# Kernel optimization log

Measured on AMD Instinct MI355X. Metric: run time of the kernel, lower is better.

## Reference

```python
import jax, jax.numpy as jnp
import numpy as np

V, E, SH, H = 30000, 1024, 2048, 1024   # vocab, emb_size, ses_hid_size, hid_size
B, T = 64, 50
PAD = 10003
H2 = 2 * H  # GRU hidden size


def setup_inputs() -> dict:
    key = jax.random.key(0)
    ks = jax.random.split(key, 12)
    s = 0.02
    emb_W = jax.random.normal(ks[2], (V, E), jnp.float32) * s
    emb_W = emb_W.at[PAD].set(0.0)  # padding_idx row is zero
    return {
        "ses_encoding": jax.random.normal(ks[0], (B, 1, SH), jnp.float32),
        "x": jax.random.randint(ks[1], (B, T), 0, V),
        "emb_W": emb_W,
        "gru_Wih": jax.random.normal(ks[3], (3 * H2, E), jnp.float32) * s,
        "gru_Whh": jax.random.normal(ks[4], (3 * H2, H2), jnp.float32) * s,
        "gru_bih": jax.random.normal(ks[5], (3 * H2,), jnp.float32) * s,
        "gru_bhh": jax.random.normal(ks[6], (3 * H2,), jnp.float32) * s,
        "lin1_W": jax.random.normal(ks[7], (H, SH), jnp.float32) * s,
        "lin1_b": jax.random.normal(ks[8], (H,), jnp.float32) * s,
        "lin2_W": jax.random.normal(ks[9], (E, H2), jnp.float32) * s,
        "lin2_b": jax.random.normal(ks[10], (E,), jnp.float32) * s,
        "out_W": jax.random.normal(ks[11], (V, E), jnp.float32) * s,
    }


def reference(ses_encoding, x, emb_W, gru_Wih, gru_Whh, gru_bih, gru_bhh,
              lin1_W, lin1_b, lin2_W, lin2_b, out_W):
    # ses_encoding: [B,1,SH] -> tanh(lin1) -> [B,1,H] -> view [1,B,H] -> [B,H]
    ses = jnp.tanh(jnp.einsum('bos,hs->boh', ses_encoding, lin1_W) + lin1_b)
    ses_enc = ses.reshape(B, H)  # [B, H]

    toks = x.T  # [T, B], teacher-forced inputs
    tok_next = jnp.concatenate([x[:, 1:], jnp.zeros((B, 1), x.dtype)], axis=1).T  # [T, B]
    has_next = jnp.arange(T) < (T - 1)  # [T]

    def step(h, xs):
        tok, nxt, hn = xs  # tok: [B]
        emb = jnp.where((tok == PAD)[:, None], 0.0, emb_W[tok])  # [B, E] (dropout=eval identity)
        hcat = jnp.concatenate([h, ses_enc], axis=-1)  # [B, 2H]
        gi = emb @ gru_Wih.T + gru_bih    # [B, 6H]
        gh = hcat @ gru_Whh.T + gru_bhh   # [B, 6H]
        i_r, i_z, i_n = jnp.split(gi, 3, axis=-1)
        h_r, h_z, h_n = jnp.split(gh, 3, axis=-1)
        r = jax.nn.sigmoid(i_r + h_r)
        z = jax.nn.sigmoid(i_z + h_z)
        n = jnp.tanh(i_n + r * h_n)
        h_full = (1.0 - z) * n + z * hcat     # [B, 2H]
        h_next = h_full[:, :H]                # keep first hid_size half
        hid_o = h_full @ lin2_W.T + lin2_b + emb  # [B, E]
        logits = hid_o @ out_W.T              # [B, V]
        logp = jax.nn.log_softmax(logits, axis=-1)
        ll = jnp.where(hn, logp[jnp.arange(B), nxt], 0.0)  # [B]
        return h_next, (logits, ll)

    _, (all_logits, all_ll) = jax.lax.scan(step, ses_enc, (toks, tok_next, has_next))
    dec_o = jnp.transpose(all_logits, (1, 0, 2))  # [B, T, V]
    log_l = jnp.sum(all_ll, axis=0)               # [B]
    return dec_o, log_l
```

## Files before the change

### kernel.cpp

```cpp
#include <hip/hip_runtime.h>
#include <hip/hip_bf16.h>
#include <stdint.h>

#define VV   30000
#define EE   1024
#define SHH  2048
#define HH   1024
#define H2   2048
#define G3   6144
#define BB   64
#define TT   50
#define PADT 10003
#define MM   3200
#define NPAD 30080
#define RBLK 64
#define PNB  (NPAD / 64)

typedef __bf16 bf16;
typedef bf16  bf16x8 __attribute__((ext_vector_type(8)));
typedef bf16  bf16x4v __attribute__((ext_vector_type(4)));
typedef float f32x4 __attribute__((ext_vector_type(4)));

__device__ __forceinline__ void async16(void* lds_base, const void* gsrc) {
    __builtin_amdgcn_global_load_lds(
        (const __attribute__((address_space(1))) void*)gsrc,
        (__attribute__((address_space(3))) void*)lds_base, 16, 0, 0);
}

__device__ __forceinline__ int xcd_swizzle(int lin, int nwg) {
    int q = nwg >> 3, r = nwg & 7;
    int x = lin & 7, o = lin >> 3;
    return (x < r ? x * (q + 1) : r * (q + 1) + (x - r) * q) + o;
}

__device__ __forceinline__ float sigmoidf_(float x) {
    return 1.f / (1.f + __expf(-x));
}

__global__ __launch_bounds__(256) void k_conv(bf16* dst, const float* src, int n) {
    int i = (blockIdx.x * 256 + threadIdx.x) * 4;
    if (i + 3 >= n) return;
    float4 v = *(const float4*)&src[i];
    bf16x4v o; o[0] = (bf16)v.x; o[1] = (bf16)v.y; o[2] = (bf16)v.z; o[3] = (bf16)v.w;
    *(bf16x4v*)&dst[i] = o;
}

__global__ __launch_bounds__(256) void k_conv_outw(bf16* dst, const float* src) {
    int row = blockIdx.x;
    int c = threadIdx.x * 4;
    bf16x4v o;
    if (row < VV) {
        float4 v = *(const float4*)&src[(size_t)row * EE + c];
        o[0] = (bf16)v.x; o[1] = (bf16)v.y; o[2] = (bf16)v.z; o[3] = (bf16)v.w;
    } else {
        o[0] = (bf16)0.f; o[1] = (bf16)0.f; o[2] = (bf16)0.f; o[3] = (bf16)0.f;
    }
    *(bf16x4v*)&dst[(size_t)row * EE + c] = o;
}

__global__ __launch_bounds__(256) void k_conv_whhhi(bf16* dst, const float* whh) {
    int d = blockIdx.x;
    int cblk = d / 192, rem = d % 192, g = rem / 64, s = rem % 64;
    const float* srow = whh + (size_t)(g * H2 + 1024 + cblk * 64 + s) * H2;
    int c = threadIdx.x * 4;
    float4 v = *(const float4*)&srow[c];
    bf16x4v o; o[0] = (bf16)v.x; o[1] = (bf16)v.y; o[2] = (bf16)v.z; o[3] = (bf16)v.w;
    *(bf16x4v*)&dst[(size_t)d * HH + c] = o;
}

__global__ __launch_bounds__(256) void k_embed(const int* x, const float* embW, bf16* out) {
    int i = blockIdx.x;
    int t = i >> 6, b = i & 63;
    int tok = x[b * TT + t];
    int e = threadIdx.x * 4;
    bf16x4v o;
    if (tok == PADT) {
        o[0] = (bf16)0.f; o[1] = (bf16)0.f; o[2] = (bf16)0.f; o[3] = (bf16)0.f;
    } else {
        float4 v = *(const float4*)&embW[(size_t)tok * EE + e];
        o[0] = (bf16)v.x; o[1] = (bf16)v.y; o[2] = (bf16)v.z; o[3] = (bf16)v.w;
    }
    *(bf16x4v*)&out[(size_t)i * EE + e] = o;
}

template<int KIND>
__global__ __launch_bounds__(256)
void sgemm64(const float* __restrict__ A, const float* __restrict__ Bm,
             const float* __restrict__ bias, float* __restrict__ Of,
             bf16* __restrict__ Ob, bf16* __restrict__ Ob2,
             int N, int K, int lda, int ldb, int koff, int ldo, int ldo2) {
    int n0 = blockIdx.x * 64;
    int tid = threadIdx.x;
    int tr = tid >> 4, tc = tid & 15;
    __shared__ float As[64][33];
    __shared__ float Bs[64][33];
    float acc[4][4] = {};
    for (int k0 = 0; k0 < K; k0 += 32) {
        #pragma unroll
        for (int q = 0; q < 8; ++q) {
            int p = q * 256 + tid; int r = p >> 5, kk = p & 31;
            As[r][kk] = A[(size_t)r * lda + k0 + kk];
            Bs[r][kk] = Bm[(size_t)(n0 + r) * ldb + koff + k0 + kk];
        }
        __syncthreads();
        #pragma unroll
        for (int kk = 0; kk < 32; ++kk) {
            float a4[4], b4[4];
            #pragma unroll
            for (int i = 0; i < 4; i++) a4[i] = As[tr * 4 + i][kk];
            #pragma unroll
            for (int j = 0; j < 4; j++) b4[j] = Bs[tc * 4 + j][kk];
            #pragma unroll
            for (int i = 0; i < 4; i++)
                #pragma unroll
                for (int j = 0; j < 4; j++) acc[i][j] += a4[i] * b4[j];
        }
        __syncthreads();
    }
    #pragma unroll
    for (int i = 0; i < 4; i++)
        #pragma unroll
        for (int j = 0; j < 4; j++) {
            int row = tr * 4 + i, col = n0 + tc * 4 + j;
            float v = acc[i][j] + bias[col];
            if (KIND == 0) {
                v = tanhf(v);
                Of[(size_t)row * N + col] = v;
                Ob[(size_t)row * ldo + col] = (bf16)v;
                Ob2[(size_t)row * ldo2 + col] = (bf16)v;
            } else {
                Of[(size_t)row * N + col] = v;
            }
        }
}

template<int KIND>
__global__ __launch_bounds__(256)
void gemm128(const bf16* __restrict__ A, const bf16* __restrict__ Bm,
             void* __restrict__ Cout, const float* __restrict__ bias,
             const bf16* __restrict__ addend, float* __restrict__ pm,
             float* __restrict__ ps, int N, int K, int lda, int ldb, int Nreal) {
    int nwg = gridDim.x * gridDim.y;
    int lin = blockIdx.y * gridDim.x + blockIdx.x;
    int wg = xcd_swizzle(lin, nwg);
    int bx = wg % gridDim.x, by = wg / gridDim.x;
    const int n0 = bx * 128;
    const int m0 = by * 128;
    const int tid = threadIdx.x;
    const int w = tid >> 6, l = tid & 63;
    const int wr = w >> 1, wc = w & 1;
    __shared__ bf16 As[2][128 * 32];
    __shared__ bf16 Bs[2][128 * 32];
    f32x4 acc[4][4] = {};
    const int lrow = l >> 2;
    const int lk = (l & 3) * 8;

    auto stage = [&](int buf, int kt) {
        #pragma unroll
        for (int q = 0; q < 2; ++q) {
            int ch = w * 2 + q;
            async16(&As[buf][ch * 512], A + (size_t)(m0 + ch * 16 + lrow) * lda + kt + lk);
            async16(&Bs[buf][ch * 512], Bm + (size_t)(n0 + ch * 16 + lrow) * ldb + kt + lk);
        }
    };

    stage(0, 0);
    __syncthreads();
    const int nk = K >> 5;
    for (int ki = 0; ki < nk; ++ki) {
        const int cur = ki & 1;
        if (ki + 1 < nk) stage(cur ^ 1, (ki + 1) << 5);
        bf16x8 af[4], bfr[4];
        #pragma unroll
        for (int mi = 0; mi < 4; mi++)
            af[mi] = *(const bf16x8*)&As[cur][(wr * 64 + mi * 16 + (l & 15)) * 32 + (l >> 4) * 8];
        #pragma unroll
        for (int ni = 0; ni < 4; ni++)
            bfr[ni] = *(const bf16x8*)&Bs[cur][(wc * 64 + ni * 16 + (l & 15)) * 32 + (l >> 4) * 8];
        #pragma unroll
        for (int mi = 0; mi < 4; mi++)
            #pragma unroll
            for (int ni = 0; ni < 4; ni++)
                acc[mi][ni] = __builtin_amdgcn_mfma_f32_16x16x32_bf16(af[mi], bfr[ni], acc[mi][ni], 0, 0, 0);
        __syncthreads();
    }
    #pragma unroll
    for (int mi = 0; mi < 4; mi++)
        #pragma unroll
        for (int ni = 0; ni < 4; ni++) {
            int row0 = m0 + wr * 64 + mi * 16 + (l >> 4) * 4;
            int col = n0 + wc * 64 + ni * 16 + (l & 15);
            f32x4 v = acc[mi][ni];
            #pragma unroll
            for (int r = 0; r < 4; r++) {
                int rr = row0 + r;
                float xv = v[r];
                if constexpr (KIND == 0 || KIND == 1) xv += bias[col];
                if constexpr (KIND == 1) xv += (float)addend[(size_t)rr * N + col];
                if constexpr (KIND == 2) {
                    if (col < Nreal) {
                        int t = rr >> 6, b = rr & 63;
                        __builtin_nontemporal_store(
                            xv, &((float*)Cout)[((size_t)(b * TT + t)) * VV + col]);
                    }
                } else {
                    ((bf16*)Cout)[(size_t)rr * N + col] = (bf16)xv;
                }
            }
        }
    if constexpr (KIND == 2) {
        #pragma unroll
        for (int mi = 0; mi < 4; mi++) {
            #pragma unroll
            for (int r = 0; r < 4; r++) {
                float m = -1e30f, s = 0.f;
                #pragma unroll
                for (int ni = 0; ni < 4; ni++) {
                    int col = n0 + wc * 64 + ni * 16 + (l & 15);
                    if (col < Nreal) {
                        float v = acc[mi][ni][r];
                        float M = fmaxf(m, v);
                        s = s * __expf(m - M) + __expf(v - M);
                        m = M;
                    }
                }
                #pragma unroll
                for (int off = 1; off < 16; off <<= 1) {
                    float m2 = __shfl_xor(m, off);
                    float s2 = __shfl_xor(s, off);
                    float M = fmaxf(m, m2);
                    s = s * __expf(m - M) + s2 * __expf(m2 - M);
                    m = M;
                }
                if ((l & 15) == 0) {
                    int row = m0 + wr * 64 + mi * 16 + (l >> 4) * 4 + r;
                    size_t pidx = (size_t)row * PNB + (n0 >> 6) + wc;
                    pm[pidx] = m; ps[pidx] = s;
                }
            }
        }
    }
}

__global__ __launch_bounds__(384, 1)
void k_rnn(const float* __restrict__ Whh,
           const bf16* __restrict__ gi_b,
           const float* __restrict__ ghs,
           bf16* __restrict__ hlo,
           bf16* __restrict__ hfx,
           uint32_t* __restrict__ ctr) {
    const int blk = blockIdx.x;
    const int c0 = blk * 16;
    const int tid = threadIdx.x;
    const int wv = tid >> 6;
    const int l  = tid & 63;
    const int g  = wv >> 1;
    const int mh = wv & 1;
    const int lc = l & 15, lk = l >> 4;
    __shared__ char h_lds[131072];
    __shared__ float ghl[3][64][17];

    bf16x8 breg[32];
    {
        const float* wrow = Whh + ((size_t)(g * H2 + c0 + lc)) * H2;
        #pragma unroll
        for (int kt = 0; kt < 32; ++kt) {
            const float* p = wrow + kt * 32 + lk * 8;
            float4 v0 = *(const float4*)p;
            float4 v1 = *(const float4*)(p + 4);
            bf16x8 o;
            o[0] = (bf16)v0.x; o[1] = (bf16)v0.y; o[2] = (bf16)v0.z; o[3] = (bf16)v0.w;
            o[4] = (bf16)v1.x; o[5] = (bf16)v1.y; o[6] = (bf16)v1.z; o[7] = (bf16)v1.w;
            breg[kt] = o;
        }
    }
    float pr[4], pz[4], pn[4];
    if (wv < 4) {
        #pragma unroll
        for (int r = 0; r < 4; ++r) {
            int b = wv * 16 + lk * 4 + r;
            size_t base = (size_t)b * G3 + c0 + lc;
            pr[r] = ghs[base];
            pz[r] = ghs[base + H2];
            pn[r] = ghs[base + 2 * H2];
        }
    }

    for (int t = 0; t < TT; ++t) {
        bf16 qr[4], qz[4], qn[4];
        if (wv < 4) {
            const bf16* gp = gi_b + ((size_t)t * BB) * G3;
            #pragma unroll
            for (int r = 0; r < 4; ++r) {
                int b = wv * 16 + lk * 4 + r;
                size_t base = (size_t)b * G3 + c0 + lc;
                qr[r] = gp[base];
                qz[r] = gp[base + H2];
                qn[r] = gp[base + 2 * H2];
            }
        }

        {
            const uint64_t* hsrc = (const uint64_t*)(hlo + (size_t)t * BB * HH);
            #pragma unroll 1
            for (int i0 = 0; i0 < 44; i0 += 22) {
                uint64_t v[22];
                #pragma unroll
                for (int j = 0; j < 22; ++j) {
                    int idx = (i0 + j) * 384 + tid;
                    if (idx < 16384)
                        v[j] = __hip_atomic_load(hsrc + idx, __ATOMIC_RELAXED,
                                                 __HIP_MEMORY_SCOPE_AGENT);
                }
                #pragma unroll
                for (int j = 0; j < 22; ++j) {
                    int idx = (i0 + j) * 384 + tid;
                    if (idx < 16384) {
                        int byte = idx * 8;
                        int swb = byte ^ (((byte >> 11) & 7) << 4);
                        *(uint64_t*)(h_lds + swb) = v[j];
                    }
                }
            }
        }
        __syncthreads();

        f32x4 acc0 = {}, acc1 = {};
        const int r0 = mh * 32 + lc, r1 = r0 + 16;
        const int sw = (lc & 7) << 4;
        #pragma unroll
        for (int kt = 0; kt < 32; ++kt) {
            int cbyte = kt * 64 + lk * 16;
            bf16x8 a0 = *(const bf16x8*)(h_lds + ((r0 * 2048 + cbyte) ^ sw));
            bf16x8 a1 = *(const bf16x8*)(h_lds + ((r1 * 2048 + cbyte) ^ sw));
            acc0 = __builtin_amdgcn_mfma_f32_16x16x32_bf16(a0, breg[kt], acc0, 0, 0, 0);
            acc1 = __builtin_amdgcn_mfma_f32_16x16x32_bf16(a1, breg[kt], acc1, 0, 0, 0);
        }
        #pragma unroll
        for (int r = 0; r < 4; ++r) {
            ghl[g][mh * 32 + lk * 4 + r][lc]      = acc0[r];
            ghl[g][mh * 32 + 16 + lk * 4 + r][lc] = acc1[r];
        }
        __syncthreads();

        if (wv < 4) {
            #pragma unroll
            for (int r = 0; r < 4; ++r) {
                int b = wv * 16 + lk * 4 + r;
                float hr = ghl[0][b][lc] + pr[r];
                float hz = ghl[1][b][lc] + pz[r];
                float hn = ghl[2][b][lc] + pn[r];
                float rg = sigmoidf_((float)qr[r] + hr);
                float zg = sigmoidf_((float)qz[r] + hz);
                float ng = tanhf((float)qn[r] + rg * hn);
                int hvb = (b * 2048 + (c0 + lc) * 2) ^ ((b & 7) << 4);
                float hv = (float)*(const bf16*)(h_lds + hvb);
                float hf = (1.f - zg) * ng + zg * hv;
                union { bf16 h; uint16_t u; } cv;
                cv.h = (bf16)hf;
                __hip_atomic_store(
                    (uint16_t*)&hlo[((size_t)(t + 1) * BB + b) * HH + c0 + lc],
                    cv.u, __ATOMIC_RELAXED, __HIP_MEMORY_SCOPE_AGENT);
                hfx[((size_t)(t + 1) * BB + b) * H2 + c0 + lc] = cv.h;
            }
        }

        if (t != TT - 1) {
            __syncthreads();
            if (tid == 0) {
                __hip_atomic_fetch_add(&ctr[t], 1u, __ATOMIC_RELAXED, __HIP_MEMORY_SCOPE_AGENT);
                while (__hip_atomic_load(&ctr[t], __ATOMIC_RELAXED, __HIP_MEMORY_SCOPE_AGENT) < RBLK)
                    __builtin_amdgcn_s_sleep(1);
            }
            __syncthreads();
        }
    }
}

__global__ __launch_bounds__(256)
void k_hi(const bf16* __restrict__ hfx_,
          const float* __restrict__ ses_f,
          const bf16* __restrict__ Wrh,
          const bf16* __restrict__ gi_b,
          const float* __restrict__ ghs,
          bf16* __restrict__ hfx_out) {
    const int cblk = blockIdx.x;
    const int t    = blockIdx.y;
    const int tid = threadIdx.x;
    const int w = tid >> 6, l = tid & 63;
    __shared__ bf16 As[64 * 32];
    __shared__ bf16 Bs[192 * 32];
    f32x4 acc[12] = {};
    const int lrow = l >> 2;
    const int lk = (l & 3) * 8;
    const bf16* Abase = hfx_ + ((size_t)t * BB) * H2;
    for (int kt = 0; kt < HH; kt += 32) {
        async16(&As[w * 512], Abase + (size_t)(w * 16 + lrow) * H2 + kt + lk);
        #pragma unroll
        for (int q = 0; q < 3; ++q) {
            int cb = w * 3 + q;
            async16(&Bs[cb * 512], Wrh + (size_t)(cblk * 192 + cb * 16 + lrow) * HH + kt + lk);
        }
        __syncthreads();
        bf16x8 af = *(const bf16x8*)&As[(w * 16 + (l & 15)) * 32 + (l >> 4) * 8];
        #pragma unroll
        for (int j = 0; j < 12; j++) {
            bf16x8 bfj = *(const bf16x8*)&Bs[(j * 16 + (l & 15)) * 32 + (l >> 4) * 8];
            acc[j] = __builtin_amdgcn_mfma_f32_16x16x32_bf16(af, bfj, acc[j], 0, 0, 0);
        }
        __syncthreads();
    }
    #pragma unroll
    for (int jc = 0; jc < 4; jc++) {
        int ch = cblk * 64 + jc * 16 + (l & 15);
        #pragma unroll
        for (int r = 0; r < 4; r++) {
            int b = w * 16 + (l >> 4) * 4 + r;
            size_t gb = (size_t)(t * BB + b) * G3 + 1024 + ch;
            size_t sb = (size_t)b * G3 + 1024 + ch;
            float gr = (float)gi_b[gb];
            float gz = (float)gi_b[gb + H2];
            float gn = (float)gi_b[gb + 2 * H2];
            float hr = acc[jc][r]     + ghs[sb];
            float hz = acc[4 + jc][r] + ghs[sb + H2];
            float hn = acc[8 + jc][r] + ghs[sb + 2 * H2];
            float rg = sigmoidf_(gr + hr);
            float zg = sigmoidf_(gz + hz);
            float ng = tanhf(gn + rg * hn);
            float hv = ses_f[b * HH + ch];
            float hf = (1.f - zg) * ng + zg * hv;
            hfx_out[((size_t)(t + 1) * BB + b) * H2 + HH + ch] = (bf16)hf;
        }
    }
}

__global__ void k_lse(const float* __restrict__ pm, const float* __restrict__ ps,
                      const float* __restrict__ logits, const int* __restrict__ x,
                      float* __restrict__ ll) {
    int row = blockIdx.x;
    int t = row >> 6, b = row & 63;
    int l = threadIdx.x;
    float m = -1e30f, s = 0.f;
    for (int i = l; i < PNB; i += 64) {
        float mi = pm[(size_t)row * PNB + i];
        float si = ps[(size_t)row * PNB + i];
        float M = fmaxf(m, mi);
        s = s * __expf(m - M) + si * __expf(mi - M);
        m = M;
    }
    #pragma unroll
    for (int off = 32; off; off >>= 1) {
        float m2 = __shfl_down(m, off);
        float s2 = __shfl_down(s, off);
        float M = fmaxf(m, m2);
        s = s * __expf(m - M) + s2 * __expf(m2 - M);
        m = M;
    }
    if (l == 0) {
        float v = 0.f;
        if (t < TT - 1) {
            int nxt = x[b * TT + t + 1];
            v = logits[((size_t)(b * TT + t)) * VV + nxt] - (m + __logf(s));
        }
        ll[row] = v;
    }
}

__global__ void k_sumll(const float* __restrict__ ll_ws, float* __restrict__ out) {
    int b = threadIdx.x;
    if (b < BB) {
        float s = 0.f;
        for (int t = 0; t < TT; t++) s += ll_ws[t * BB + b];
        out[b] = s;
    }
}

extern "C" void kernel_launch(void* const* d_in, const int* in_sizes, int n_in,
                              void* d_out, int out_size, void* d_ws, size_t ws_size,
                              hipStream_t stream) {
    const float* ses_encoding = (const float*)d_in[0];
    const int*   x            = (const int*)d_in[1];
    const float* emb_W        = (const float*)d_in[2];
    const float* gru_Wih      = (const float*)d_in[3];
    const float* gru_Whh      = (const float*)d_in[4];
    const float* gru_bih      = (const float*)d_in[5];
    const float* gru_bhh      = (const float*)d_in[6];
    const float* lin1_W       = (const float*)d_in[7];
    const float* lin1_b       = (const float*)d_in[8];
    const float* lin2_W       = (const float*)d_in[9];
    const float* lin2_b       = (const float*)d_in[10];
    const float* out_W        = (const float*)d_in[11];

    char* W = (char*)d_ws;
    size_t off = 0;
    auto take = [&](size_t bytes) { void* p = W + off; off += (bytes + 255) & ~(size_t)255; return p; };

    float* ses_f32 = (float*)take((size_t)BB * HH * 4);
    bf16* Wih_b    = (bf16*)take((size_t)G3 * EE * 2);
    bf16* Wrh_b    = (bf16*)take((size_t)3072 * HH * 2);
    bf16* lin2_b16 = (bf16*)take((size_t)EE * H2 * 2);
    bf16* outW_b   = (bf16*)take((size_t)NPAD * EE * 2);
    bf16* emb_b    = (bf16*)take((size_t)MM * EE * 2);
    bf16* gi_b     = (bf16*)take((size_t)MM * G3 * 2);
    float* ghs     = (float*)take((size_t)BB * G3 * 4);
    bf16* hlo      = (bf16*)take((size_t)(TT + 1) * BB * HH * 2);
    bf16* hfx      = (bf16*)take((size_t)(TT + 1) * BB * H2 * 2);
    bf16* hido_b   = (bf16*)take((size_t)MM * EE * 2);
    float* ll_ws   = (float*)take((size_t)MM * 4);
    float* pm      = (float*)take((size_t)MM * PNB * 4);
    float* ps      = (float*)take((size_t)MM * PNB * 4);
    uint32_t* ctr  = (uint32_t*)take((size_t)TT * 4);

    hipMemsetAsync(ctr, 0, (size_t)TT * 4, stream);

    k_conv<<<(G3 * EE) / 1024, 256, 0, stream>>>(Wih_b, gru_Wih, G3 * EE);
    k_conv<<<(EE * H2) / 1024, 256, 0, stream>>>(lin2_b16, lin2_W, EE * H2);
    k_conv_outw<<<NPAD, 256, 0, stream>>>(outW_b, out_W);
    k_conv_whhhi<<<3072, 256, 0, stream>>>(Wrh_b, gru_Whh);
    k_embed<<<MM, 256, 0, stream>>>(x, emb_W, emb_b);

    sgemm64<0><<<HH / 64, 256, 0, stream>>>(ses_encoding, lin1_W, lin1_b, ses_f32,
                                            hfx, hlo, HH, SHH, SHH, SHH, 0, H2, HH);
    sgemm64<1><<<G3 / 64, 256, 0, stream>>>(ses_f32, gru_Whh, gru_bhh, ghs, nullptr,
                                            nullptr, G3, HH, HH, H2, HH, 0, 0);

    gemm128<0><<<dim3(G3 / 128, MM / 128), 256, 0, stream>>>(
        emb_b, Wih_b, gi_b, gru_bih, nullptr, nullptr, nullptr, G3, EE, EE, EE, 0);

    k_rnn<<<RBLK, 384, 0, stream>>>(gru_Whh, gi_b, ghs, hlo, hfx, ctr);

    k_hi<<<dim3(16, TT), 256, 0, stream>>>(hfx, ses_f32, Wrh_b, gi_b, ghs, hfx);

    gemm128<1><<<dim3(EE / 128, MM / 128), 256, 0, stream>>>(
        hfx + (size_t)BB * H2, lin2_b16, hido_b, lin2_b, emb_b, nullptr, nullptr,
        EE, H2, H2, H2, 0);

    gemm128<2><<<dim3(NPAD / 128, MM / 128), 256, 0, stream>>>(
        hido_b, outW_b, d_out, nullptr, nullptr, pm, ps, NPAD, EE, EE, EE, VV);

    k_lse<<<MM, 64, 0, stream>>>(pm, ps, (const float*)d_out, x, ll_ws);
    k_sumll<<<1, 64, 0, stream>>>(ll_ws, (float*)d_out + (size_t)BB * TT * VV);
}
```

Measured before the change: 1.508 ms.

## Fuse upper-half GRU gate kernel into recurrent kernel as overlapping worker blocks

The separate k_hi launch is merged into k_rnn. 192 extra blocks poll the per-step counters and compute the upper-half hidden GEMM and gates for each finished timestep while the 64 recurrent blocks continue with later steps. The aim is to hide k_hi's work behind the serial recurrence and remove one launch. The cost is that the worker blocks share the GPU with the recurrent blocks and spin on flags. Only 4 of their 6 waves do work, and both block types reserve the large LDS allocation, so each takes a whole CU.

```diff
diff --git a/kernel.cpp b/kernel.cpp
--- a/kernel.cpp
+++ b/kernel.cpp
@@ -14,6 +14,7 @@
 #define MM   3200
 #define NPAD 30080
 #define RBLK 64
+#define HIBLK 192
 #define PNB  (NPAD / 64)
 
 typedef __bf16 bf16;
@@ -248,188 +249,203 @@
            const float* __restrict__ ghs,
            bf16* __restrict__ hlo,
            bf16* __restrict__ hfx,
-           uint32_t* __restrict__ ctr) {
-    const int blk = blockIdx.x;
-    const int c0 = blk * 16;
+           uint32_t* __restrict__ ctr,
+           const float* __restrict__ ses_f,
+           const bf16* __restrict__ Wrh) {
+    __shared__ char smem[144128];
     const int tid = threadIdx.x;
     const int wv = tid >> 6;
     const int l  = tid & 63;
-    const int g  = wv >> 1;
-    const int mh = wv & 1;
-    const int lc = l & 15, lk = l >> 4;
-    __shared__ char h_lds[131072];
-    __shared__ float ghl[3][64][17];
-
-    bf16x8 breg[32];
-    {
-        const float* wrow = Whh + ((size_t)(g * H2 + c0 + lc)) * H2;
-        #pragma unroll
-        for (int kt = 0; kt < 32; ++kt) {
-            const float* p = wrow + kt * 32 + lk * 8;
-            float4 v0 = *(const float4*)p;
-            float4 v1 = *(const float4*)(p + 4);
-            bf16x8 o;
-            o[0] = (bf16)v0.x; o[1] = (bf16)v0.y; o[2] = (bf16)v0.z; o[3] = (bf16)v0.w;
-            o[4] = (bf16)v1.x; o[5] = (bf16)v1.y; o[6] = (bf16)v1.z; o[7] = (bf16)v1.w;
-            breg[kt] = o;
-        }
-    }
-    float pr[4], pz[4], pn[4];
-    if (wv < 4) {
-        #pragma unroll
-        for (int r = 0; r < 4; ++r) {
-            int b = wv * 16 + lk * 4 + r;
-            size_t base = (size_t)b * G3 + c0 + lc;
-            pr[r] = ghs[base];
-            pz[r] = ghs[base + H2];
-            pn[r] = ghs[base + 2 * H2];
-        }
-    }
-
-    for (int t = 0; t < TT; ++t) {
-        bf16 qr[4], qz[4], qn[4];
+
+    if (blockIdx.x < RBLK) {
+        char* h_lds = smem;
+        float (*ghl)[64][17] = (float(*)[64][17])(smem + 131072);
+        const int blk = blockIdx.x;
+        const int c0 = blk * 16;
+        const int g  = wv >> 1;
+        const int mh = wv & 1;
+        const int lc = l & 15, lk = l >> 4;
+
+        bf16x8 breg[32];
+        {
+            const float* wrow = Whh + ((size_t)(g * H2 + c0 + lc)) * H2;
+            #pragma unroll
+            for (int kt = 0; kt < 32; ++kt) {
+                const float* p = wrow + kt * 32 + lk * 8;
+                float4 v0 = *(const float4*)p;
+                float4 v1 = *(const float4*)(p + 4);
+                bf16x8 o;
+                o[0] = (bf16)v0.x; o[1] = (bf16)v0.y; o[2] = (bf16)v0.z; o[3] = (bf16)v0.w;
+                o[4] = (bf16)v1.x; o[5] = (bf16)v1.y; o[6] = (bf16)v1.z; o[7] = (bf16)v1.w;
+                breg[kt] = o;
+            }
+        }
+        float pr[4], pz[4], pn[4];
         if (wv < 4) {
-            const bf16* gp = gi_b + ((size_t)t * BB) * G3;
             #pragma unroll
             for (int r = 0; r < 4; ++r) {
                 int b = wv * 16 + lk * 4 + r;
                 size_t base = (size_t)b * G3 + c0 + lc;
-                qr[r] = gp[base];
-                qz[r] = gp[base + H2];
-                qn[r] = gp[base + 2 * H2];
-            }
-        }
-
-        {
-            const uint64_t* hsrc = (const uint64_t*)(hlo + (size_t)t * BB * HH);
-            #pragma unroll 1
-            for (int i0 = 0; i0 < 44; i0 += 22) {
-                uint64_t v[22];
+                pr[r] = ghs[base];
+                pz[r] = ghs[base + H2];
+                pn[r] = ghs[base + 2 * H2];
+            }
+        }
+
+        for (int t = 0; t < TT; ++t) {
+            bf16 qr[4], qz[4], qn[4];
+            if (wv < 4) {
+                const bf16* gp = gi_b + ((size_t)t * BB) * G3;
                 #pragma unroll
-                for (int j = 0; j < 22; ++j) {
-                    int idx = (i0 + j) * 384 + tid;
-                    if (idx < 16384)
-                        v[j] = __hip_atomic_load(hsrc + idx, __ATOMIC_RELAXED,
-                                                 __HIP_MEMORY_SCOPE_AGENT);
-                }
+                for (int r = 0; r < 4; ++r) {
+                    int b = wv * 16 + lk * 4 + r;
+                    size_t base = (size_t)b * G3 + c0 + lc;
+                    qr[r] = gp[base];
+                    qz[r] = gp[base + H2];
+                    qn[r] = gp[base + 2 * H2];
+                }
+            }
+            {
+                const uint64_t* hsrc = (const uint64_t*)(hlo + (size_t)t * BB * HH);
+                #pragma unroll 1
+                for (int i0 = 0; i0 < 44; i0 += 22) {
+                    uint64_t v[22];
+                    #pragma unroll
+                    for (int j = 0; j < 22; ++j) {
+                        int idx = (i0 + j) * 384 + tid;
+                        if (idx < 16384)
+                            v[j] = __hip_atomic_load(hsrc + idx, __ATOMIC_RELAXED,
+                                                     __HIP_MEMORY_SCOPE_AGENT);
+                    }
+                    #pragma unroll
+                    for (int j = 0; j < 22; ++j) {
+                        int idx = (i0 + j) * 384 + tid;
+                        if (idx < 16384) {
+                            int byte = idx * 8;
+                            int swb = byte ^ (((byte >> 11) & 7) << 4);
+                            *(uint64_t*)(h_lds + swb) = v[j];
+                        }
+                    }
+                }
+            }
+            __syncthreads();
+
+            f32x4 acc0 = {}, acc1 = {};
+            const int r0 = mh * 32 + lc, r1 = r0 + 16;
+            const int sw = (lc & 7) << 4;
+            #pragma unroll
+            for (int kt = 0; kt < 32; ++kt) {
+                int cbyte = kt * 64 + lk * 16;
+                bf16x8 a0 = *(const bf16x8*)(h_lds + ((r0 * 2048 + cbyte) ^ sw));
+                bf16x8 a1 = *(const bf16x8*)(h_lds + ((r1 * 2048 + cbyte) ^ sw));
+                acc0 = __builtin_amdgcn_mfma_f32_16x16x32_bf16(a0, breg[kt], acc0, 0, 0, 0);
+                acc1 = __builtin_amdgcn_mfma_f32_16x16x32_bf16(a1, breg[kt], acc1, 0, 0, 0);
+            }
+            #pragma unroll
+            for (int r = 0; r < 4; ++r) {
+                ghl[g][mh * 32 + lk * 4 + r][lc]      = acc0[r];
+                ghl[g][mh * 32 + 16 + lk * 4 + r][lc] = acc1[r];
+            }
+            __syncthreads();
+
+            if (wv < 4) {
                 #pragma unroll
-                for (int j = 0; j < 22; ++j) {
-                    int idx = (i0 + j) * 384 + tid;
-                    if (idx < 16384) {
-                        int byte = idx * 8;
-                        int swb = byte ^ (((byte >> 11) & 7) << 4);
-                        *(uint64_t*)(h_lds + swb) = v[j];
-                    }
-                }
-            }
-        }
-        __syncthreads();
-
-        f32x4 acc0 = {}, acc1 = {};
-        const int r0 = mh * 32 + lc, r1 = r0 + 16;
-        const int sw = (lc & 7) << 4;
-        #pragma unroll
-        for (int kt = 0; kt < 32; ++kt) {
-            int cbyte = kt * 64 + lk * 16;
-            bf16x8 a0 = *(const bf16x8*)(h_lds + ((r0 * 2048 + cbyte) ^ sw));
-            bf16x8 a1 = *(const bf16x8*)(h_lds + ((r1 * 2048 + cbyte) ^ sw));
-            acc0 = __builtin_amdgcn_mfma_f32_16x16x32_bf16(a0, breg[kt], acc0, 0, 0, 0);
-            acc1 = __builtin_amdgcn_mfma_f32_16x16x32_bf16(a1, breg[kt], acc1, 0, 0, 0);
-        }
-        #pragma unroll
-        for (int r = 0; r < 4; ++r) {
-            ghl[g][mh * 32 + lk * 4 + r][lc]      = acc0[r];
-            ghl[g][mh * 32 + 16 + lk * 4 + r][lc] = acc1[r];
-        }
-        __syncthreads();
-
-        if (wv < 4) {
-            #pragma unroll
-            for (int r = 0; r < 4; ++r) {
-                int b = wv * 16 + lk * 4 + r;
-                float hr = ghl[0][b][lc] + pr[r];
-                float hz = ghl[1][b][lc] + pz[r];
-                float hn = ghl[2][b][lc] + pn[r];
-                float rg = sigmoidf_((float)qr[r] + hr);
-                float zg = sigmoidf_((float)qz[r] + hz);
-                float ng = tanhf((float)qn[r] + rg * hn);
-                int hvb = (b * 2048 + (c0 + lc) * 2) ^ ((b & 7) << 4);
-                float hv = (float)*(const bf16*)(h_lds + hvb);
-                float hf = (1.f - zg) * ng + zg * hv;
-                union { bf16 h; uint16_t u; } cv;
-                cv.h = (bf16)hf;
-                __hip_atomic_store(
-                    (uint16_t*)&hlo[((size_t)(t + 1) * BB + b) * HH + c0 + lc],
-                    cv.u, __ATOMIC_RELAXED, __HIP_MEMORY_SCOPE_AGENT);
-                hfx[((size_t)(t + 1) * BB + b) * H2 + c0 + lc] = cv.h;
-            }
-        }
-
-        if (t != TT - 1) {
+                for (int r = 0; r < 4; ++r) {
+                    int b = wv * 16 + lk * 4 + r;
+                    float hr = ghl[0][b][lc] + pr[r];
+                    float hz = ghl[1][b][lc] + pz[r];
+                    float hn = ghl[2][b][lc] + pn[r];
+                    float rg = sigmoidf_((float)qr[r] + hr);
+                    float zg = sigmoidf_((float)qz[r] + hz);
+                    float ng = tanhf((float)qn[r] + rg * hn);
+                    int hvb = (b * 2048 + (c0 + lc) * 2) ^ ((b & 7) << 4);
+                    float hv = (float)*(const bf16*)(h_lds + hvb);
+                    float hf = (1.f - zg) * ng + zg * hv;
+                    union { bf16 h; uint16_t u; } cv;
+                    cv.h = (bf16)hf;
+                    __hip_atomic_store(
+                        (uint16_t*)&hlo[((size_t)(t + 1) * BB + b) * HH + c0 + lc],
+                        cv.u, __ATOMIC_RELAXED, __HIP_MEMORY_SCOPE_AGENT);
+                    hfx[((size_t)(t + 1) * BB + b) * H2 + c0 + lc] = cv.h;
+                }
+            }
+
+            if (t != TT - 1) {
+                __syncthreads();
+                if (tid == 0) {
+                    __hip_atomic_fetch_add(&ctr[t], 1u, __ATOMIC_RELAXED, __HIP_MEMORY_SCOPE_AGENT);
+                    while (__hip_atomic_load(&ctr[t], __ATOMIC_RELAXED, __HIP_MEMORY_SCOPE_AGENT) < RBLK)
+                        __builtin_amdgcn_s_sleep(1);
+                }
+                __syncthreads();
+            }
+        }
+    } else {
+        bf16* As = (bf16*)smem;
+        bf16* Bs = (bf16*)(smem + 4096);
+        const int w = wv;
+        const int lrow = l >> 2;
+        const int lk8 = (l & 3) * 8;
+
+        for (int item = (int)blockIdx.x - RBLK; item < TT * 16; item += HIBLK) {
+            const int t = item >> 4, cblk = item & 15;
+            if (t > 0 && tid == 0) {
+                while (__hip_atomic_load(&ctr[t - 1], __ATOMIC_RELAXED, __HIP_MEMORY_SCOPE_AGENT) < RBLK)
+                    __builtin_amdgcn_s_sleep(32);
+            }
             __syncthreads();
-            if (tid == 0) {
-                __hip_atomic_fetch_add(&ctr[t], 1u, __ATOMIC_RELAXED, __HIP_MEMORY_SCOPE_AGENT);
-                while (__hip_atomic_load(&ctr[t], __ATOMIC_RELAXED, __HIP_MEMORY_SCOPE_AGENT) < RBLK)
-                    __builtin_amdgcn_s_sleep(1);
+
+            f32x4 acc[12] = {};
+            for (int kt = 0; kt < HH; kt += 32) {
+                if (w < 4) {
+                    const uint64_t* src = (const uint64_t*)(
+                        hlo + ((size_t)t * BB + w * 16 + lrow) * HH + kt + lk8);
+                    uint64_t v0 = __hip_atomic_load(src, __ATOMIC_RELAXED, __HIP_MEMORY_SCOPE_AGENT);
+                    uint64_t v1 = __hip_atomic_load(src + 1, __ATOMIC_RELAXED, __HIP_MEMORY_SCOPE_AGENT);
+                    uint64_t* dst = (uint64_t*)((char*)As + w * 1024 + l * 16);
+                    dst[0] = v0; dst[1] = v1;
+                    #pragma unroll
+                    for (int q = 0; q < 3; ++q) {
+                        int cb = w * 3 + q;
+                        async16(&Bs[cb * 512], Wrh + (size_t)(cblk * 192 + cb * 16 + lrow) * HH + kt + lk8);
+                    }
+                }
+                __syncthreads();
+                if (w < 4) {
+                    bf16x8 af = *(const bf16x8*)&As[(w * 16 + (l & 15)) * 32 + (l >> 4) * 8];
+                    #pragma unroll
+                    for (int j = 0; j < 12; j++) {
+                        bf16x8 bfj = *(const bf16x8*)&Bs[(j * 16 + (l & 15)) * 32 + (l >> 4) * 8];
+                        acc[j] = __builtin_amdgcn_mfma_f32_16x16x32_bf16(af, bfj, acc[j], 0, 0, 0);
+                    }
+                }
+                __syncthreads();
+            }
+            if (w < 4) {
+                #pragma unroll
+                for (int jc = 0; jc < 4; jc++) {
+                    int ch = cblk * 64 + jc * 16 + (l & 15);
+                    #pragma unroll
+                    for (int r = 0; r < 4; r++) {
+                        int b = w * 16 + (l >> 4) * 4 + r;
+                        size_t gb = (size_t)(t * BB + b) * G3 + 1024 + ch;
+                        size_t sb = (size_t)b * G3 + 1024 + ch;
+                        float gr = (float)gi_b[gb];
+                        float gz = (float)gi_b[gb + H2];
+                        float gn = (float)gi_b[gb + 2 * H2];
+                        float hr = acc[jc][r]     + ghs[sb];
+                        float hz = acc[4 + jc][r] + ghs[sb + H2];
+                        float hn = acc[8 + jc][r] + ghs[sb + 2 * H2];
+                        float rg = sigmoidf_(gr + hr);
+                        float zg = sigmoidf_(gz + hz);
+                        float ng = tanhf(gn + rg * hn);
+                        float hv = ses_f[b * HH + ch];
+                        float hf = (1.f - zg) * ng + zg * hv;
+                        hfx[((size_t)(t + 1) * BB + b) * H2 + HH + ch] = (bf16)hf;
+                    }
+                }
             }
             __syncthreads();
-        }
-    }
-}
-
-__global__ __launch_bounds__(256)
-void k_hi(const bf16* __restrict__ hfx_,
-          const float* __restrict__ ses_f,
-          const bf16* __restrict__ Wrh,
-          const bf16* __restrict__ gi_b,
-          const float* __restrict__ ghs,
-          bf16* __restrict__ hfx_out) {
-    const int cblk = blockIdx.x;
-    const int t    = blockIdx.y;
-    const int tid = threadIdx.x;
-    const int w = tid >> 6, l = tid & 63;
-    __shared__ bf16 As[64 * 32];
-    __shared__ bf16 Bs[192 * 32];
-    f32x4 acc[12] = {};
-    const int lrow = l >> 2;
-    const int lk = (l & 3) * 8;
-    const bf16* Abase = hfx_ + ((size_t)t * BB) * H2;
-    for (int kt = 0; kt < HH; kt += 32) {
-        async16(&As[w * 512], Abase + (size_t)(w * 16 + lrow) * H2 + kt + lk);
-        #pragma unroll
-        for (int q = 0; q < 3; ++q) {
-            int cb = w * 3 + q;
-            async16(&Bs[cb * 512], Wrh + (size_t)(cblk * 192 + cb * 16 + lrow) * HH + kt + lk);
-        }
-        __syncthreads();
-        bf16x8 af = *(const bf16x8*)&As[(w * 16 + (l & 15)) * 32 + (l >> 4) * 8];
-        #pragma unroll
-        for (int j = 0; j < 12; j++) {
-            bf16x8 bfj = *(const bf16x8*)&Bs[(j * 16 + (l & 15)) * 32 + (l >> 4) * 8];
-            acc[j] = __builtin_amdgcn_mfma_f32_16x16x32_bf16(af, bfj, acc[j], 0, 0, 0);
-        }
-        __syncthreads();
-    }
-    #pragma unroll
-    for (int jc = 0; jc < 4; jc++) {
-        int ch = cblk * 64 + jc * 16 + (l & 15);
-        #pragma unroll
-        for (int r = 0; r < 4; r++) {
-            int b = w * 16 + (l >> 4) * 4 + r;
-            size_t gb = (size_t)(t * BB + b) * G3 + 1024 + ch;
-            size_t sb = (size_t)b * G3 + 1024 + ch;
-            float gr = (float)gi_b[gb];
-            float gz = (float)gi_b[gb + H2];
-            float gn = (float)gi_b[gb + 2 * H2];
-            float hr = acc[jc][r]     + ghs[sb];
-            float hz = acc[4 + jc][r] + ghs[sb + H2];
-            float hn = acc[8 + jc][r] + ghs[sb + 2 * H2];
-            float rg = sigmoidf_(gr + hr);
-            float zg = sigmoidf_(gz + hz);
-            float ng = tanhf(gn + rg * hn);
-            float hv = ses_f[b * HH + ch];
-            float hf = (1.f - zg) * ng + zg * hv;
-            hfx_out[((size_t)(t + 1) * BB + b) * H2 + HH + ch] = (bf16)hf;
         }
     }
 }
@@ -527,9 +543,8 @@
     gemm128<0><<<dim3(G3 / 128, MM / 128), 256, 0, stream>>>(
         emb_b, Wih_b, gi_b, gru_bih, nullptr, nullptr, nullptr, G3, EE, EE, EE, 0);
 
-    k_rnn<<<RBLK, 384, 0, stream>>>(gru_Whh, gi_b, ghs, hlo, hfx, ctr);
-
-    k_hi<<<dim3(16, TT), 256, 0, stream>>>(hfx, ses_f32, Wrh_b, gi_b, ghs, hfx);
+    k_rnn<<<RBLK + HIBLK, 384, 0, stream>>>(gru_Whh, gi_b, ghs, hlo, hfx, ctr,
+                                            ses_f32, Wrh_b);
 
     gemm128<1><<<dim3(EE / 128, MM / 128), 256, 0, stream>>>(
         hfx + (size_t)BB * H2, lin2_b16, hido_b, lin2_b, emb_b, nullptr, nullptr,
```

New measurement: 1.581 ms. 4.8% more time.

## Halve recurrent blocks, widen each to 32 columns, async-copy hidden state into LDS

Applied to the files above, without the earlier changes.

The persistent GRU recurrence kernel now runs 32 blocks of 768 threads, each covering 32 hidden columns instead of 16. This halves the number of blocks taking part in the per-timestep grid barrier and halves the total redundant reads of the hidden state. The per-step hidden-state load now uses global_load_lds direct-to-LDS copies with the swizzle applied on the source address, replacing relaxed atomic loads staged through registers. The trade-offs are fewer CUs active on the serial recurrence, and the risk that the non-atomic async loads see stale data written by other blocks on other XCDs.

```diff
diff --git a/kernel.cpp b/kernel.cpp
--- a/kernel.cpp
+++ b/kernel.cpp
@@ -13,7 +13,7 @@
 #define PADT 10003
 #define MM   3200
 #define NPAD 30080
-#define RBLK 64
+#define RBLK 32
 #define PNB  (NPAD / 64)
 
 typedef __bf16 bf16;
@@ -242,7 +242,7 @@
     }
 }
 
-__global__ __launch_bounds__(384, 1)
+__global__ __launch_bounds__(768, 1)
 void k_rnn(const float* __restrict__ Whh,
            const bf16* __restrict__ gi_b,
            const float* __restrict__ ghs,
@@ -250,19 +250,21 @@
            bf16* __restrict__ hfx,
            uint32_t* __restrict__ ctr) {
     const int blk = blockIdx.x;
-    const int c0 = blk * 16;
+    const int c0 = blk * 32;
     const int tid = threadIdx.x;
     const int wv = tid >> 6;
     const int l  = tid & 63;
-    const int g  = wv >> 1;
+    const int rowgroup = wv >> 1;
+    const int g  = rowgroup >> 1;
+    const int ch = rowgroup & 1;
     const int mh = wv & 1;
     const int lc = l & 15, lk = l >> 4;
     __shared__ char h_lds[131072];
-    __shared__ float ghl[3][64][17];
+    __shared__ float ghl[3][64][33];
 
     bf16x8 breg[32];
     {
-        const float* wrow = Whh + ((size_t)(g * H2 + c0 + lc)) * H2;
+        const float* wrow = Whh + ((size_t)(g * H2 + c0 + ch * 16 + lc)) * H2;
         #pragma unroll
         for (int kt = 0; kt < 32; ++kt) {
             const float* p = wrow + kt * 32 + lk * 8;
@@ -274,12 +276,14 @@
             breg[kt] = o;
         }
     }
+    const int eb0 = (wv >> 1) * 16;
+    const int ec  = c0 + (wv & 1) * 16 + lc;
     float pr[4], pz[4], pn[4];
-    if (wv < 4) {
+    if (wv < 8) {
         #pragma unroll
         for (int r = 0; r < 4; ++r) {
-            int b = wv * 16 + lk * 4 + r;
-            size_t base = (size_t)b * G3 + c0 + lc;
+            int b = eb0 + lk * 4 + r;
+            size_t base = (size_t)b * G3 + ec;
             pr[r] = ghs[base];
             pz[r] = ghs[base + H2];
             pn[r] = ghs[base + 2 * H2];
@@ -288,12 +292,12 @@
 
     for (int t = 0; t < TT; ++t) {
         bf16 qr[4], qz[4], qn[4];
-        if (wv < 4) {
+        if (wv < 8) {
             const bf16* gp = gi_b + ((size_t)t * BB) * G3;
             #pragma unroll
             for (int r = 0; r < 4; ++r) {
-                int b = wv * 16 + lk * 4 + r;
-                size_t base = (size_t)b * G3 + c0 + lc;
+                int b = eb0 + lk * 4 + r;
+                size_t base = (size_t)b * G3 + ec;
                 qr[r] = gp[base];
                 qz[r] = gp[base + H2];
                 qn[r] = gp[base + 2 * H2];
@@ -301,25 +305,14 @@
         }
 
         {
-            const uint64_t* hsrc = (const uint64_t*)(hlo + (size_t)t * BB * HH);
-            #pragma unroll 1
-            for (int i0 = 0; i0 < 44; i0 += 22) {
-                uint64_t v[22];
-                #pragma unroll
-                for (int j = 0; j < 22; ++j) {
-                    int idx = (i0 + j) * 384 + tid;
-                    if (idx < 16384)
-                        v[j] = __hip_atomic_load(hsrc + idx, __ATOMIC_RELAXED,
-                                                 __HIP_MEMORY_SCOPE_AGENT);
-                }
-                #pragma unroll
-                for (int j = 0; j < 22; ++j) {
-                    int idx = (i0 + j) * 384 + tid;
-                    if (idx < 16384) {
-                        int byte = idx * 8;
-                        int swb = byte ^ (((byte >> 11) & 7) << 4);
-                        *(uint64_t*)(h_lds + swb) = v[j];
-                    }
+            const char* hbase = (const char*)(hlo + (size_t)t * BB * HH);
+            #pragma unroll
+            for (int it = 0; it < 11; ++it) {
+                int cbase = it * 768 + wv * 64;
+                if (cbase + 64 <= 8192) {
+                    int B = (cbase + l) * 16;
+                    const char* src = hbase + (B ^ (((B >> 11) & 7) << 4));
+                    async16(h_lds + cbase * 16, src);
                 }
             }
         }
@@ -338,30 +331,31 @@
         }
         #pragma unroll
         for (int r = 0; r < 4; ++r) {
-            ghl[g][mh * 32 + lk * 4 + r][lc]      = acc0[r];
-            ghl[g][mh * 32 + 16 + lk * 4 + r][lc] = acc1[r];
-        }
-        __syncthreads();
-
-        if (wv < 4) {
+            ghl[g][mh * 32 + lk * 4 + r][ch * 16 + lc]      = acc0[r];
+            ghl[g][mh * 32 + 16 + lk * 4 + r][ch * 16 + lc] = acc1[r];
+        }
+        __syncthreads();
+
+        if (wv < 8) {
+            const int cc = (wv & 1) * 16 + lc;
             #pragma unroll
             for (int r = 0; r < 4; ++r) {
-                int b = wv * 16 + lk * 4 + r;
-                float hr = ghl[0][b][lc] + pr[r];
-                float hz = ghl[1][b][lc] + pz[r];
-                float hn = ghl[2][b][lc] + pn[r];
+                int b = eb0 + lk * 4 + r;
+                float hr = ghl[0][b][cc] + pr[r];
+                float hz = ghl[1][b][cc] + pz[r];
+                float hn = ghl[2][b][cc] + pn[r];
                 float rg = sigmoidf_((float)qr[r] + hr);
                 float zg = sigmoidf_((float)qz[r] + hz);
                 float ng = tanhf((float)qn[r] + rg * hn);
-                int hvb = (b * 2048 + (c0 + lc) * 2) ^ ((b & 7) << 4);
+                int hvb = (b * 2048 + ec * 2) ^ ((b & 7) << 4);
                 float hv = (float)*(const bf16*)(h_lds + hvb);
                 float hf = (1.f - zg) * ng + zg * hv;
                 union { bf16 h; uint16_t u; } cv;
                 cv.h = (bf16)hf;
                 __hip_atomic_store(
-                    (uint16_t*)&hlo[((size_t)(t + 1) * BB + b) * HH + c0 + lc],
+                    (uint16_t*)&hlo[((size_t)(t + 1) * BB + b) * HH + ec],
                     cv.u, __ATOMIC_RELAXED, __HIP_MEMORY_SCOPE_AGENT);
-                hfx[((size_t)(t + 1) * BB + b) * H2 + c0 + lc] = cv.h;
+                hfx[((size_t)(t + 1) * BB + b) * H2 + ec] = cv.h;
             }
         }
 
@@ -527,7 +521,7 @@
     gemm128<0><<<dim3(G3 / 128, MM / 128), 256, 0, stream>>>(
         emb_b, Wih_b, gi_b, gru_bih, nullptr, nullptr, nullptr, G3, EE, EE, EE, 0);
 
-    k_rnn<<<RBLK, 384, 0, stream>>>(gru_Whh, gi_b, ghs, hlo, hfx, ctr);
+    k_rnn<<<RBLK, 768, 0, stream>>>(gru_Whh, gi_b, ghs, hlo, hfx, ctr);
 
     k_hi<<<dim3(16, TT), 256, 0, stream>>>(hfx, ses_f32, Wrh_b, gi_b, ghs, hfx);
 
```

Result: slower. 1.714 ms (+13.7%).
